# Kernel optimization log

Measured on AMD Instinct MI355X. Metric: run time of the kernel, lower is better.

The kernel has to match this reference:

```python
import jax, jax.numpy as jnp
import numpy as np

B, N, DIM = 2, 2048, 2048
HEADS, DIM_HEAD = 16, 64
INNER = HEADS * DIM_HEAD  # 1024, != DIM -> to_out projection active
SCALE = DIM_HEAD ** -0.5


def setup_inputs() -> dict:
    key = jax.random.key(0)
    ks = jax.random.split(key, 10)
    s_in = 1.0 / np.sqrt(DIM)
    s_out = 1.0 / np.sqrt(INNER)
    return {
        "h_t": jax.random.normal(ks[0], (B, N, DIM), jnp.float32),
        "h_a": jax.random.normal(ks[1], (B, N, DIM), jnp.float32),
        "h_v": jax.random.normal(ks[2], (B, N, DIM), jnp.float32),
        "W_q": jax.random.normal(ks[3], (DIM, INNER), jnp.float32) * s_in,
        "W_k_ta": jax.random.normal(ks[4], (DIM, INNER), jnp.float32) * s_in,
        "W_k_tv": jax.random.normal(ks[5], (DIM, INNER), jnp.float32) * s_in,
        "W_v_ta": jax.random.normal(ks[6], (DIM, INNER), jnp.float32) * s_in,
        "W_v_tv": jax.random.normal(ks[7], (DIM, INNER), jnp.float32) * s_in,
        "W_out": jax.random.normal(ks[8], (INNER, DIM), jnp.float32) * s_out,
        "b_out": jnp.zeros((DIM,), jnp.float32),
    }


def _split_heads(x):
    # [b, n, h*d] -> [b, h, n, d]
    b, n, _ = x.shape
    return x.reshape(b, n, HEADS, DIM_HEAD).transpose(0, 2, 1, 3)


def _cross_attn(q, k, v):
    # q,k,v: [b, h, n, d]
    dots = jnp.einsum('bhid,bhjd->bhij', q, k) * SCALE
    attn = jax.nn.softmax(dots, axis=-1)
    out = jnp.einsum('bhij,bhjd->bhid', attn, v)
    b, h, n, d = out.shape
    return out.transpose(0, 2, 1, 3).reshape(b, n, h * d)  # [b, n, h*d]


def reference(h_t, h_a, h_v, W_q, W_k_ta, W_k_tv, W_v_ta, W_v_tv, W_out, b_out):
    q = _split_heads(h_t @ W_q)
    k_ta = _split_heads(h_a @ W_k_ta)
    v_ta = _split_heads(h_a @ W_v_ta)
    k_tv = _split_heads(h_v @ W_k_tv)
    v_tv = _split_heads(h_v @ W_v_tv)
    out_ta = _cross_attn(q, k_ta, v_ta)
    out_tv = _cross_attn(q, k_tv, v_tv)
    # project_out=True since inner_dim != dim; dropout=0 (eval)
    return h_t + (out_ta + out_tv) @ W_out + b_out
```

## Files before the change

kernel.cpp:

```cpp
#include <hip/hip_runtime.h>
#include <hip/hip_bf16.h>

typedef __attribute__((ext_vector_type(8))) short s16x8;
typedef __attribute__((ext_vector_type(4))) float f32x4;
typedef unsigned short u16;
typedef unsigned int u32;
typedef unsigned long long u64;

__device__ __forceinline__ u16 f2bf(float x) {
  __hip_bfloat16 h = __float2bfloat16(x);
  return *reinterpret_cast<u16*>(&h);
}
__device__ __forceinline__ float bf2f(u16 x) {
  union { u32 u; float f; } c; c.u = ((u32)x) << 16; return c.f;
}
__device__ __forceinline__ u32 pk2(float lo, float hi) {
  return ((u32)f2bf(hi) << 16) | (u32)f2bf(lo);
}

__device__ __forceinline__ void glds16(const void* g, void* lds) {
  __builtin_amdgcn_global_load_lds(
      (const __attribute__((address_space(1))) u32*)(u64)g,
      (__attribute__((address_space(3))) u32*)(u32)(u64)lds, 16, 0, 0);
}

__device__ __forceinline__ void tcast_tile(const float* __restrict__ in,
                                           u16* __restrict__ out,
                                           int R, int C, int ldo,
                                           int bx, int by, int tid,
                                           u16 (*t)[72]) {
  const int c0 = bx * 64, r0 = by * 64;
#pragma unroll
  for (int it = 0; it < 4; ++it) {
    int c = it * 256 + tid;
    int row = c >> 4, sub = c & 15;
    float4 v = *(const float4*)(in + (u64)(r0 + row) * C + c0 + sub * 4);
    t[sub * 4 + 0][row] = f2bf(v.x);
    t[sub * 4 + 1][row] = f2bf(v.y);
    t[sub * 4 + 2][row] = f2bf(v.z);
    t[sub * 4 + 3][row] = f2bf(v.w);
  }
  __syncthreads();
#pragma unroll
  for (int it = 0; it < 2; ++it) {
    int c = it * 256 + tid;
    int orow = c >> 3, osub = c & 7;
    *(s16x8*)(out + (u64)(c0 + orow) * ldo + r0 + osub * 8) =
        *(const s16x8*)&t[orow][osub * 8];
  }
}

__global__ __launch_bounds__(256) void k_prep(
    const float* __restrict__ h_t, const float* __restrict__ h_a,
    const float* __restrict__ h_v, const float* __restrict__ W_q,
    const float* __restrict__ W_k_ta, const float* __restrict__ W_v_ta,
    const float* __restrict__ W_k_tv, const float* __restrict__ W_v_tv,
    const float* __restrict__ W_out, u16* __restrict__ hT,
    u16* __restrict__ hA, u16* __restrict__ hV, u16* __restrict__ WqT,
    u16* __restrict__ WkvTa, u16* __restrict__ WkvTv, u16* __restrict__ WoT) {
  __shared__ u16 t[64][72];
  const int bid = blockIdx.x, tid = threadIdx.x;
  if (bid < 12288) {
    const float* in = bid < 4096 ? h_t : bid < 8192 ? h_a : h_v;
    u16* out = bid < 4096 ? hT : bid < 8192 ? hA : hV;
    const int i = (bid & 4095) * 2048 + tid * 8;
    float4 a = *(const float4*)(in + i);
    float4 b = *(const float4*)(in + i + 4);
    union { s16x8 v; u16 e[8]; } r;
    r.e[0] = f2bf(a.x); r.e[1] = f2bf(a.y); r.e[2] = f2bf(a.z); r.e[3] = f2bf(a.w);
    r.e[4] = f2bf(b.x); r.e[5] = f2bf(b.y); r.e[6] = f2bf(b.z); r.e[7] = f2bf(b.w);
    *(s16x8*)(out + i) = r.v;
  } else if (bid < 14848) {
    const int tt = bid - 12288;
    const int wi = tt / 512, t2 = tt % 512;
    const float* in;
    u16* out;
    switch (wi) {
      case 0: in = W_q;    out = WqT; break;
      case 1: in = W_k_ta; out = WkvTa; break;
      case 2: in = W_v_ta; out = WkvTa + 1024 * 2048; break;
      case 3: in = W_k_tv; out = WkvTv; break;
      default: in = W_v_tv; out = WkvTv + 1024 * 2048; break;
    }
    tcast_tile(in, out, 2048, 1024, 2048, t2 % 16, t2 / 16, tid, t);
  } else {
    const int t2 = bid - 14848;
    tcast_tile(W_out, WoT, 1024, 2048, 1024, t2 % 32, t2 / 32, tid, t);
  }
}

__global__ __launch_bounds__(256) void k_vtrans2(const u16* __restrict__ kva,
                                                 const u16* __restrict__ kvv,
                                                 u16* __restrict__ vta,
                                                 u16* __restrict__ vtv) {
  __shared__ u16 t[64][72];
  const int bx = blockIdx.x, tb = blockIdx.y;
  const int bh = bx & 31;
  const u16* kv = (bx < 32) ? kva : kvv;
  u16* vt = (bx < 32) ? vta : vtv;
  const int b = bh >> 4, h = bh & 15;
  const int tid = threadIdx.x;
  const u16* src = kv + (u64)(b * 2048 + tb * 64) * 2048 + 1024 + h * 64;
#pragma unroll
  for (int it = 0; it < 2; ++it) {
    int c = it * 256 + tid;
    int trow = c >> 3, dsub = c & 7;
    union { s16x8 v; u16 e[8]; } u;
    u.v = *(const s16x8*)(src + (u64)trow * 2048 + dsub * 8);
#pragma unroll
    for (int j = 0; j < 8; ++j) t[dsub * 8 + j][trow] = u.e[j];
  }
  __syncthreads();
  u16* dst = vt + (u64)bh * 64 * 2048 + tb * 64;
#pragma unroll
  for (int it = 0; it < 2; ++it) {
    int c = it * 256 + tid;
    int drow = c >> 3, tsub = c & 7;
    *(s16x8*)(dst + (u64)drow * 2048 + tsub * 8) = *(const s16x8*)&t[drow][tsub * 8];
  }
}

__global__ __launch_bounds__(256) void k_add(const u16* __restrict__ ao,
                                             u16* __restrict__ aoc) {
  const int i = blockIdx.x * 2048 + threadIdx.x * 8;
  const int row = i >> 10, col = i & 1023;
  union { s16x8 v; u16 e[8]; } A, B, O;
  A.v = *(const s16x8*)(ao + (u64)row * 2048 + col);
  B.v = *(const s16x8*)(ao + (u64)row * 2048 + 1024 + col);
#pragma unroll
  for (int j = 0; j < 8; ++j) O.e[j] = f2bf(bf2f(A.e[j]) + bf2f(B.e[j]));
  *(s16x8*)(aoc + (u64)row * 1024 + col) = O.v;
}

template <int TM, int TN, int MODE>
__device__ __forceinline__ void gemm_body(const u16* __restrict__ A,
                                          const u16* __restrict__ Bt,
                                          void* __restrict__ Cout,
                                          const float* __restrict__ resid,
                                          const float* __restrict__ bias,
                                          int M, int N, int K, float scale,
                                          int bxx, int byy) {
  constexpr int MR = TM / 32, NR = TN / 32;
  __shared__ u16 smem[(TM + TN) * 64];
  const int tid = threadIdx.x;
  const int lane = tid & 63, w = tid >> 6;
  const int g = lane >> 4, lr = lane & 15;
  const int wm = (w >> 1) * (TM / 2), wn = (w & 1) * (TN / 2);
  const int m0 = byy * TM, n0 = bxx * TN;

  f32x4 acc[MR][NR] = {};
  int roff[2];
  roff[0] = (g * 16) ^ ((lr & 7) << 4);
  roff[1] = (64 + g * 16) ^ ((lr & 7) << 4);

  const int nkt = K >> 6;
  for (int kt = 0; kt < nkt; ++kt) {
    const int k0 = kt << 6;
#pragma unroll
    for (int it = 0; it < (TM + TN) / 32; ++it) {
      int c = it * 256 + tid;
      int p = c * 16;
      const u16* gsrc;
      if (c < TM * 8) {
        int lby = p ^ (((p >> 7) & 7) << 4);
        gsrc = A + (u64)(m0 + (lby >> 7)) * K + k0 + ((lby >> 4) & 7) * 8;
      } else {
        int pb = p - TM * 128;
        int lby = pb ^ (((pb >> 7) & 7) << 4);
        gsrc = Bt + (u64)(n0 + (lby >> 7)) * K + k0 + ((lby >> 4) & 7) * 8;
      }
      glds16(gsrc, (char*)smem + p);
    }
    __syncthreads();
#pragma unroll
    for (int ks = 0; ks < 2; ++ks) {
      s16x8 a[MR], b[NR];
#pragma unroll
      for (int m = 0; m < MR; ++m)
        a[m] = *(const s16x8*)((const char*)smem + (wm + m * 16 + lr) * 128 + roff[ks]);
#pragma unroll
      for (int n = 0; n < NR; ++n)
        b[n] = *(const s16x8*)((const char*)smem + TM * 128 + (wn + n * 16 + lr) * 128 + roff[ks]);
#pragma unroll
      for (int m = 0; m < MR; ++m)
#pragma unroll
        for (int n = 0; n < NR; ++n)
          acc[m][n] = __builtin_amdgcn_mfma_f32_16x16x32_bf16(a[m], b[n], acc[m][n], 0, 0, 0);
    }
    __syncthreads();
  }

#pragma unroll
  for (int m = 0; m < MR; ++m)
#pragma unroll
    for (int n = 0; n < NR; ++n) {
      const int col = n0 + wn + n * 16 + lr;
#pragma unroll
      for (int r = 0; r < 4; ++r) {
        const int row = m0 + wm + m * 16 + g * 4 + r;
        if constexpr (MODE == 0) {
          ((u16*)Cout)[(u64)row * N + col] = f2bf(acc[m][n][r]);
        } else if constexpr (MODE == 2) {
          ((u16*)Cout)[(u64)row * N + col] = f2bf(acc[m][n][r] * scale);
        } else {
          ((float*)Cout)[(u64)row * N + col] =
              acc[m][n][r] + resid[(u64)row * N + col] + bias[col];
        }
      }
    }
}

template <int TM, int TN, int MODE>
__global__ __launch_bounds__(256) void k_gemm(const u16* __restrict__ A,
                                              const u16* __restrict__ Bt,
                                              void* __restrict__ Cout,
                                              const float* __restrict__ resid,
                                              const float* __restrict__ bias,
                                              int M, int N, int K, float scale) {
  gemm_body<TM, TN, MODE>(A, Bt, Cout, resid, bias, M, N, K, scale,
                          blockIdx.x, blockIdx.y);
}

__global__ __launch_bounds__(256) void k_gemm_kv(const u16* __restrict__ A0,
                                                 const u16* __restrict__ A1,
                                                 const u16* __restrict__ B0,
                                                 const u16* __restrict__ B1,
                                                 u16* __restrict__ C0,
                                                 u16* __restrict__ C1) {
  const int z = blockIdx.z;
  gemm_body<128, 128, 0>(z ? A1 : A0, z ? B1 : B0, z ? C1 : C0,
                         nullptr, nullptr, 4096, 2048, 2048, 1.0f,
                         blockIdx.x, blockIdx.y);
}

__global__ __launch_bounds__(512, 6) void k_attn(const u16* __restrict__ Q,
                                                 const u16* __restrict__ Kta,
                                                 const u16* __restrict__ Ktv,
                                                 const u16* __restrict__ VTta,
                                                 const u16* __restrict__ VTtv,
                                                 u16* __restrict__ AO) {
  const int bx = blockIdx.x;
  const int br = bx & 1, bh = bx >> 1;
  const int b = bh >> 4, h = bh & 15;
  const int qb = blockIdx.y;
  const int tid = threadIdx.x, lane = tid & 63, w = tid >> 6;
  const int g = lane >> 4, q = lane & 15;
  const int qrow = b * 2048 + qb * 128 + w * 16;
  const int bh64 = bh * 64;
  const u16* Kp  = br ? Ktv  : Kta;
  const u16* VTp = br ? VTtv : VTta;

  __shared__ __align__(16) char sbuf[2][16384];
  __shared__ u32 pbuf[8][16][32];

  s16x8 qf[2];
#pragma unroll
  for (int ks = 0; ks < 2; ++ks)
    qf[ks] = *(const s16x8*)(Q + (u64)(qrow + q) * 1024 + h * 64 + ks * 32 + g * 8);

  union { s16x8 v; u16 e[8]; } ones;
#pragma unroll
  for (int j = 0; j < 8; ++j) ones.e[j] = 0x3F80;

  const int sp = tid * 16;
  const int slby = sp ^ (((sp >> 7) & 7) << 4);
  const int srow = slby >> 7, scol = (slby & 127) >> 1;

  {
    glds16(Kp + (u64)(b * 2048 + srow) * 2048 + h * 64 + scol, sbuf[0] + sp);
    glds16(VTp + (u64)(bh64 + srow) * 2048 + scol, sbuf[0] + 8192 + sp);
  }
  __syncthreads();

  f32x4 lacc = {};
  f32x4 acco[4] = {};
  const int xsw = (q & 7) << 4;
  const int psw = (q & 7) << 2;

  for (int t = 0; t < 32; ++t) {
    const int cur = t & 1;
    if (t + 1 < 32) {
      const int kv1 = (t + 1) * 64;
      glds16(Kp + (u64)(b * 2048 + kv1 + srow) * 2048 + h * 64 + scol,
             sbuf[cur ^ 1] + sp);
      glds16(VTp + (u64)(bh64 + srow) * 2048 + kv1 + scol,
             sbuf[cur ^ 1] + 8192 + sp);
    }

    f32x4 s[4];
    __builtin_amdgcn_s_setprio(1);
#pragma unroll
    for (int n = 0; n < 4; ++n) {
      const char* base = sbuf[cur] + (16 * n + q) * 128;
      s16x8 kf0 = *(const s16x8*)(base + ((16 * g) ^ xsw));
      s16x8 kf1 = *(const s16x8*)(base + ((64 + 16 * g) ^ xsw));
      f32x4 z = {};
      z = __builtin_amdgcn_mfma_f32_16x16x32_bf16(kf0, qf[0], z, 0, 0, 0);
      s[n] = __builtin_amdgcn_mfma_f32_16x16x32_bf16(kf1, qf[1], z, 0, 0, 0);
    }
    __builtin_amdgcn_s_setprio(0);

#pragma unroll
    for (int n = 0; n < 4; ++n) {
#pragma unroll
      for (int r = 0; r < 4; ++r) s[n][r] = __builtin_amdgcn_exp2f(s[n][r]);
      pbuf[w][q][(8 * n + 2 * g) ^ psw]     = pk2(s[n][0], s[n][1]);
      pbuf[w][q][(8 * n + 2 * g + 1) ^ psw] = pk2(s[n][2], s[n][3]);
    }
    s16x8 pb[2];
#pragma unroll
    for (int ks = 0; ks < 2; ++ks)
      pb[ks] = *(const s16x8*)&pbuf[w][q][(16 * ks + 4 * g) ^ psw];

    __builtin_amdgcn_s_setprio(1);
    lacc = __builtin_amdgcn_mfma_f32_16x16x32_bf16(ones.v, pb[0], lacc, 0, 0, 0);
    lacc = __builtin_amdgcn_mfma_f32_16x16x32_bf16(ones.v, pb[1], lacc, 0, 0, 0);
#pragma unroll
    for (int n = 0; n < 4; ++n) {
      const char* base = sbuf[cur] + 8192 + (16 * n + q) * 128;
      s16x8 v0 = *(const s16x8*)(base + ((16 * g) ^ xsw));
      s16x8 v1 = *(const s16x8*)(base + ((64 + 16 * g) ^ xsw));
      acco[n] = __builtin_amdgcn_mfma_f32_16x16x32_bf16(v0, pb[0], acco[n], 0, 0, 0);
      acco[n] = __builtin_amdgcn_mfma_f32_16x16x32_bf16(v1, pb[1], acco[n], 0, 0, 0);
    }
    __builtin_amdgcn_s_setprio(0);
    __syncthreads();
  }

  const float inv = 1.0f / lacc[0];

#pragma unroll
  for (int n = 0; n < 4; ++n) {
    pbuf[w][q][(8 * n + 2 * g) ^ psw]     = pk2(acco[n][0] * inv, acco[n][1] * inv);
    pbuf[w][q][(8 * n + 2 * g + 1) ^ psw] = pk2(acco[n][2] * inv, acco[n][3] * inv);
  }
#pragma unroll
  for (int c = 0; c < 2; ++c) {
    const int row = (lane >> 3) + 8 * c;
    const int wc = (lane & 7) * 4;
    s16x8 vv = *(const s16x8*)&pbuf[w][row][wc ^ ((row & 7) << 2)];
    *(s16x8*)(AO + (u64)(b * 2048 + qb * 128 + w * 16 + row) * 2048 +
              br * 1024 + h * 64 + (lane & 7) * 8) = vv;
  }
}

extern "C" void kernel_launch(void* const* d_in, const int* in_sizes, int n_in,
                              void* d_out, int out_size, void* d_ws, size_t ws_size,
                              hipStream_t stream) {
  (void)in_sizes; (void)n_in; (void)out_size; (void)ws_size;
  const float* h_t    = (const float*)d_in[0];
  const float* h_a    = (const float*)d_in[1];
  const float* h_v    = (const float*)d_in[2];
  const float* W_q    = (const float*)d_in[3];
  const float* W_k_ta = (const float*)d_in[4];
  const float* W_k_tv = (const float*)d_in[5];
  const float* W_v_ta = (const float*)d_in[6];
  const float* W_v_tv = (const float*)d_in[7];
  const float* W_out  = (const float*)d_in[8];
  const float* b_out  = (const float*)d_in[9];
  float* out = (float*)d_out;

  const float CEXP = 0.125f * 1.44269504088896f;

  u16* ws    = (u16*)d_ws;
  u16* hT    = ws;
  u16* hA    = hT + 8388608;
  u16* hV    = hA + 8388608;
  u16* WqT   = hV + 8388608;
  u16* WkvTa = WqT + 2097152;
  u16* WkvTv = WkvTa + 4194304;
  u16* WoT   = WkvTv + 4194304;
  u16* Qb    = WoT + 2097152;
  u16* KVta  = Qb + 4194304;
  u16* KVtv  = KVta + 8388608;
  u16* VTta  = KVtv + 8388608;
  u16* VTtv  = VTta + 4194304;
  u16* AO    = hT;
  u16* AOc   = hA;

  k_prep<<<15360, 256, 0, stream>>>(h_t, h_a, h_v, W_q, W_k_ta, W_v_ta,
                                    W_k_tv, W_v_tv, W_out,
                                    hT, hA, hV, WqT, WkvTa, WkvTv, WoT);

  k_gemm<64, 128, 2><<<dim3(8, 64), 256, 0, stream>>>(hT, WqT, Qb, nullptr, nullptr, 4096, 1024, 2048, CEXP);
  k_gemm_kv<<<dim3(16, 32, 2), 256, 0, stream>>>(hA, hV, WkvTa, WkvTv, KVta, KVtv);

  k_vtrans2<<<dim3(64, 32), 256, 0, stream>>>(KVta, KVtv, VTta, VTtv);

  k_attn<<<dim3(64, 16), 512, 0, stream>>>(Qb, KVta, KVtv, VTta, VTtv, AO);

  k_add<<<2048, 256, 0, stream>>>(AO, AOc);

  k_gemm<128, 128, 1><<<dim3(16, 32), 256, 0, stream>>>(AOc, WoT, out, h_t, b_out, 4096, 2048, 1024, 1.0f);
}
```

Before: 294.2 us.

## Fuse head-branch sum into output GEMM and merge Q/KV projection launches

Removes the standalone k_add kernel. The output-projection GEMM (new MODE 3) now loads both branch halves of the attention output, adds them in registers and writes the sum to shared memory, instead of staging a pre-summed buffer through global memory. The Q projection is also folded into the KV projection launch as a third z-slice using 128x128 tiles; the surplus x-blocks of that slice return early. This saves a kernel launch and a global round-trip of the summed buffer. In exchange, the A-operand load in the output GEMM becomes a register load plus add instead of a direct global-to-LDS copy, and the Q GEMM uses larger tiles, which gives fewer blocks.

```diff
diff --git a/kernel.cpp b/kernel.cpp
--- a/kernel.cpp
+++ b/kernel.cpp
@@ -120,18 +120,6 @@
   }
 }
 
-__global__ __launch_bounds__(256) void k_add(const u16* __restrict__ ao,
-                                             u16* __restrict__ aoc) {
-  const int i = blockIdx.x * 2048 + threadIdx.x * 8;
-  const int row = i >> 10, col = i & 1023;
-  union { s16x8 v; u16 e[8]; } A, B, O;
-  A.v = *(const s16x8*)(ao + (u64)row * 2048 + col);
-  B.v = *(const s16x8*)(ao + (u64)row * 2048 + 1024 + col);
-#pragma unroll
-  for (int j = 0; j < 8; ++j) O.e[j] = f2bf(bf2f(A.e[j]) + bf2f(B.e[j]));
-  *(s16x8*)(aoc + (u64)row * 1024 + col) = O.v;
-}
-
 template <int TM, int TN, int MODE>
 __device__ __forceinline__ void gemm_body(const u16* __restrict__ A,
                                           const u16* __restrict__ Bt,
@@ -160,16 +148,26 @@
     for (int it = 0; it < (TM + TN) / 32; ++it) {
       int c = it * 256 + tid;
       int p = c * 16;
-      const u16* gsrc;
       if (c < TM * 8) {
         int lby = p ^ (((p >> 7) & 7) << 4);
-        gsrc = A + (u64)(m0 + (lby >> 7)) * K + k0 + ((lby >> 4) & 7) * 8;
+        if constexpr (MODE == 3) {
+          const u16* g0 = A + (u64)(m0 + (lby >> 7)) * 2048 + k0 + ((lby >> 4) & 7) * 8;
+          union { s16x8 v; u16 e[8]; } a0, a1, r;
+          a0.v = *(const s16x8*)g0;
+          a1.v = *(const s16x8*)(g0 + 1024);
+#pragma unroll
+          for (int j = 0; j < 8; ++j) r.e[j] = f2bf(bf2f(a0.e[j]) + bf2f(a1.e[j]));
+          *(s16x8*)((char*)smem + p) = r.v;
+        } else {
+          glds16(A + (u64)(m0 + (lby >> 7)) * K + k0 + ((lby >> 4) & 7) * 8,
+                 (char*)smem + p);
+        }
       } else {
         int pb = p - TM * 128;
         int lby = pb ^ (((pb >> 7) & 7) << 4);
-        gsrc = Bt + (u64)(n0 + (lby >> 7)) * K + k0 + ((lby >> 4) & 7) * 8;
+        glds16(Bt + (u64)(n0 + (lby >> 7)) * K + k0 + ((lby >> 4) & 7) * 8,
+               (char*)smem + p);
       }
-      glds16(gsrc, (char*)smem + p);
     }
     __syncthreads();
 #pragma unroll
@@ -221,16 +219,24 @@
                           blockIdx.x, blockIdx.y);
 }
 
-__global__ __launch_bounds__(256) void k_gemm_kv(const u16* __restrict__ A0,
-                                                 const u16* __restrict__ A1,
-                                                 const u16* __restrict__ B0,
-                                                 const u16* __restrict__ B1,
-                                                 u16* __restrict__ C0,
-                                                 u16* __restrict__ C1) {
+__global__ __launch_bounds__(256) void k_gemm_qkv(
+    const u16* __restrict__ hT, const u16* __restrict__ hA,
+    const u16* __restrict__ hV, const u16* __restrict__ WqT,
+    const u16* __restrict__ WkvTa, const u16* __restrict__ WkvTv,
+    u16* __restrict__ Qb, u16* __restrict__ KVta, u16* __restrict__ KVtv,
+    float cexp) {
   const int z = blockIdx.z;
-  gemm_body<128, 128, 0>(z ? A1 : A0, z ? B1 : B0, z ? C1 : C0,
-                         nullptr, nullptr, 4096, 2048, 2048, 1.0f,
-                         blockIdx.x, blockIdx.y);
+  if (z == 0) {
+    if (blockIdx.x >= 8) return;
+    gemm_body<128, 128, 2>(hT, WqT, Qb, nullptr, nullptr,
+                           4096, 1024, 2048, cexp, blockIdx.x, blockIdx.y);
+  } else if (z == 1) {
+    gemm_body<128, 128, 0>(hA, WkvTa, KVta, nullptr, nullptr,
+                           4096, 2048, 2048, 1.0f, blockIdx.x, blockIdx.y);
+  } else {
+    gemm_body<128, 128, 0>(hV, WkvTv, KVtv, nullptr, nullptr,
+                           4096, 2048, 2048, 1.0f, blockIdx.x, blockIdx.y);
+  }
 }
 
 __global__ __launch_bounds__(512, 6) void k_attn(const u16* __restrict__ Q,
@@ -376,20 +382,17 @@
   u16* VTta  = KVtv + 8388608;
   u16* VTtv  = VTta + 4194304;
   u16* AO    = hT;
-  u16* AOc   = hA;
 
   k_prep<<<15360, 256, 0, stream>>>(h_t, h_a, h_v, W_q, W_k_ta, W_v_ta,
                                     W_k_tv, W_v_tv, W_out,
                                     hT, hA, hV, WqT, WkvTa, WkvTv, WoT);
 
-  k_gemm<64, 128, 2><<<dim3(8, 64), 256, 0, stream>>>(hT, WqT, Qb, nullptr, nullptr, 4096, 1024, 2048, CEXP);
-  k_gemm_kv<<<dim3(16, 32, 2), 256, 0, stream>>>(hA, hV, WkvTa, WkvTv, KVta, KVtv);
+  k_gemm_qkv<<<dim3(16, 32, 3), 256, 0, stream>>>(hT, hA, hV, WqT, WkvTa,
+                                                  WkvTv, Qb, KVta, KVtv, CEXP);
 
   k_vtrans2<<<dim3(64, 32), 256, 0, stream>>>(KVta, KVtv, VTta, VTtv);
 
   k_attn<<<dim3(64, 16), 512, 0, stream>>>(Qb, KVta, KVtv, VTta, VTtv, AO);
 
-  k_add<<<2048, 256, 0, stream>>>(AO, AOc);
-
-  k_gemm<128, 128, 1><<<dim3(16, 32), 256, 0, stream>>>(AOc, WoT, out, h_t, b_out, 4096, 2048, 1024, 1.0f);
-}
+  k_gemm<128, 128, 3><<<dim3(16, 32), 256, 0, stream>>>(AO, WoT, out, h_t, b_out, 4096, 2048, 1024, 1.0f);
+}
```

Result: slower. 309.3 us (+5.1%).

## Compute transposed V directly via swapped-operand GEMM, dropping the transpose kernel

Applied to the files above, without the earlier changes.

The fused K/V projection GEMM is split in two. K is computed alone into a compact 1024-wide buffer, and V^T is produced directly by a second GEMM that swaps operands (W_v^T times h^T), writing with a new per-batch output layout. This removes the separate V transpose kernel and its extra write and read of the V activations. The attention kernel's K stride is updated to match. The cost is one more GEMM launch, and the V^T GEMM now stores with a different write pattern.

```diff
diff --git a/kernel.cpp b/kernel.cpp
--- a/kernel.cpp
+++ b/kernel.cpp
@@ -89,37 +89,6 @@
   }
 }
 
-__global__ __launch_bounds__(256) void k_vtrans2(const u16* __restrict__ kva,
-                                                 const u16* __restrict__ kvv,
-                                                 u16* __restrict__ vta,
-                                                 u16* __restrict__ vtv) {
-  __shared__ u16 t[64][72];
-  const int bx = blockIdx.x, tb = blockIdx.y;
-  const int bh = bx & 31;
-  const u16* kv = (bx < 32) ? kva : kvv;
-  u16* vt = (bx < 32) ? vta : vtv;
-  const int b = bh >> 4, h = bh & 15;
-  const int tid = threadIdx.x;
-  const u16* src = kv + (u64)(b * 2048 + tb * 64) * 2048 + 1024 + h * 64;
-#pragma unroll
-  for (int it = 0; it < 2; ++it) {
-    int c = it * 256 + tid;
-    int trow = c >> 3, dsub = c & 7;
-    union { s16x8 v; u16 e[8]; } u;
-    u.v = *(const s16x8*)(src + (u64)trow * 2048 + dsub * 8);
-#pragma unroll
-    for (int j = 0; j < 8; ++j) t[dsub * 8 + j][trow] = u.e[j];
-  }
-  __syncthreads();
-  u16* dst = vt + (u64)bh * 64 * 2048 + tb * 64;
-#pragma unroll
-  for (int it = 0; it < 2; ++it) {
-    int c = it * 256 + tid;
-    int drow = c >> 3, tsub = c & 7;
-    *(s16x8*)(dst + (u64)drow * 2048 + tsub * 8) = *(const s16x8*)&t[drow][tsub * 8];
-  }
-}
-
 __global__ __launch_bounds__(256) void k_add(const u16* __restrict__ ao,
                                              u16* __restrict__ aoc) {
   const int i = blockIdx.x * 2048 + threadIdx.x * 8;
@@ -202,6 +171,10 @@
           ((u16*)Cout)[(u64)row * N + col] = f2bf(acc[m][n][r]);
         } else if constexpr (MODE == 2) {
           ((u16*)Cout)[(u64)row * N + col] = f2bf(acc[m][n][r] * scale);
+        } else if constexpr (MODE == 4) {
+          const int bb = col >> 11;
+          ((u16*)Cout)[(u64)bb * 2097152 + (u64)row * 2048 + (col & 2047)] =
+              f2bf(acc[m][n][r]);
         } else {
           ((float*)Cout)[(u64)row * N + col] =
               acc[m][n][r] + resid[(u64)row * N + col] + bias[col];
@@ -221,15 +194,27 @@
                           blockIdx.x, blockIdx.y);
 }
 
-__global__ __launch_bounds__(256) void k_gemm_kv(const u16* __restrict__ A0,
+__global__ __launch_bounds__(256) void k_gemm_k(const u16* __restrict__ A0,
+                                                const u16* __restrict__ A1,
+                                                const u16* __restrict__ B0,
+                                                const u16* __restrict__ B1,
+                                                u16* __restrict__ C0,
+                                                u16* __restrict__ C1) {
+  const int z = blockIdx.z;
+  gemm_body<128, 128, 0>(z ? A1 : A0, z ? B1 : B0, z ? C1 : C0,
+                         nullptr, nullptr, 4096, 1024, 2048, 1.0f,
+                         blockIdx.x, blockIdx.y);
+}
+
+__global__ __launch_bounds__(256) void k_gemm_vt(const u16* __restrict__ A0,
                                                  const u16* __restrict__ A1,
                                                  const u16* __restrict__ B0,
                                                  const u16* __restrict__ B1,
                                                  u16* __restrict__ C0,
                                                  u16* __restrict__ C1) {
   const int z = blockIdx.z;
-  gemm_body<128, 128, 0>(z ? A1 : A0, z ? B1 : B0, z ? C1 : C0,
-                         nullptr, nullptr, 4096, 2048, 2048, 1.0f,
+  gemm_body<128, 128, 4>(z ? A1 : A0, z ? B1 : B0, z ? C1 : C0,
+                         nullptr, nullptr, 1024, 4096, 2048, 1.0f,
                          blockIdx.x, blockIdx.y);
 }
 
@@ -267,7 +252,7 @@
   const int srow = slby >> 7, scol = (slby & 127) >> 1;
 
   {
-    glds16(Kp + (u64)(b * 2048 + srow) * 2048 + h * 64 + scol, sbuf[0] + sp);
+    glds16(Kp + (u64)(b * 2048 + srow) * 1024 + h * 64 + scol, sbuf[0] + sp);
     glds16(VTp + (u64)(bh64 + srow) * 2048 + scol, sbuf[0] + 8192 + sp);
   }
   __syncthreads();
@@ -281,7 +266,7 @@
     const int cur = t & 1;
     if (t + 1 < 32) {
       const int kv1 = (t + 1) * 64;
-      glds16(Kp + (u64)(b * 2048 + kv1 + srow) * 2048 + h * 64 + scol,
+      glds16(Kp + (u64)(b * 2048 + kv1 + srow) * 1024 + h * 64 + scol,
              sbuf[cur ^ 1] + sp);
       glds16(VTp + (u64)(bh64 + srow) * 2048 + kv1 + scol,
              sbuf[cur ^ 1] + 8192 + sp);
@@ -371,9 +356,9 @@
   u16* WkvTv = WkvTa + 4194304;
   u16* WoT   = WkvTv + 4194304;
   u16* Qb    = WoT + 2097152;
-  u16* KVta  = Qb + 4194304;
-  u16* KVtv  = KVta + 8388608;
-  u16* VTta  = KVtv + 8388608;
+  u16* Kta   = Qb + 4194304;
+  u16* Ktv   = Kta + 4194304;
+  u16* VTta  = Ktv + 4194304;
   u16* VTtv  = VTta + 4194304;
   u16* AO    = hT;
   u16* AOc   = hA;
@@ -383,11 +368,13 @@
                                     hT, hA, hV, WqT, WkvTa, WkvTv, WoT);
 
   k_gemm<64, 128, 2><<<dim3(8, 64), 256, 0, stream>>>(hT, WqT, Qb, nullptr, nullptr, 4096, 1024, 2048, CEXP);
-  k_gemm_kv<<<dim3(16, 32, 2), 256, 0, stream>>>(hA, hV, WkvTa, WkvTv, KVta, KVtv);
-
-  k_vtrans2<<<dim3(64, 32), 256, 0, stream>>>(KVta, KVtv, VTta, VTtv);
-
-  k_attn<<<dim3(64, 16), 512, 0, stream>>>(Qb, KVta, KVtv, VTta, VTtv, AO);
+
+  k_gemm_k<<<dim3(8, 32, 2), 256, 0, stream>>>(hA, hV, WkvTa, WkvTv, Kta, Ktv);
+
+  k_gemm_vt<<<dim3(32, 8, 2), 256, 0, stream>>>(WkvTa + 1024 * 2048, WkvTv + 1024 * 2048,
+                                                hA, hV, VTta, VTtv);
+
+  k_attn<<<dim3(64, 16), 512, 0, stream>>>(Qb, Kta, Ktv, VTta, VTtv, AO);
 
   k_add<<<2048, 256, 0, stream>>>(AO, AOc);
 
```

Result: slower. 301.4 us (+2.4%).

## Fuse both cross-attention branches into one attention block and drop add kernel

Applied to the files above, without the earlier changes.

Each attention block now loops over both the text-audio and text-video branches in sequence, sums the normalized outputs in registers, and writes the combined bf16 result directly. This removes the separate elementwise add kernel and the round trip of the doubled-width intermediate buffer. The cost is that the grid is halved (512 blocks instead of 1024), so each block runs twice as long and there is less parallelism across the GPU. The running sum is also held in extra registers, which may affect occupancy.

```diff
diff --git a/kernel.cpp b/kernel.cpp
--- a/kernel.cpp
+++ b/kernel.cpp
@@ -120,18 +120,6 @@
   }
 }
 
-__global__ __launch_bounds__(256) void k_add(const u16* __restrict__ ao,
-                                             u16* __restrict__ aoc) {
-  const int i = blockIdx.x * 2048 + threadIdx.x * 8;
-  const int row = i >> 10, col = i & 1023;
-  union { s16x8 v; u16 e[8]; } A, B, O;
-  A.v = *(const s16x8*)(ao + (u64)row * 2048 + col);
-  B.v = *(const s16x8*)(ao + (u64)row * 2048 + 1024 + col);
-#pragma unroll
-  for (int j = 0; j < 8; ++j) O.e[j] = f2bf(bf2f(A.e[j]) + bf2f(B.e[j]));
-  *(s16x8*)(aoc + (u64)row * 1024 + col) = O.v;
-}
-
 template <int TM, int TN, int MODE>
 __device__ __forceinline__ void gemm_body(const u16* __restrict__ A,
                                           const u16* __restrict__ Bt,
@@ -238,17 +226,14 @@
                                                  const u16* __restrict__ Ktv,
                                                  const u16* __restrict__ VTta,
                                                  const u16* __restrict__ VTtv,
-                                                 u16* __restrict__ AO) {
-  const int bx = blockIdx.x;
-  const int br = bx & 1, bh = bx >> 1;
+                                                 u16* __restrict__ AOc) {
+  const int bh = blockIdx.x;
   const int b = bh >> 4, h = bh & 15;
   const int qb = blockIdx.y;
   const int tid = threadIdx.x, lane = tid & 63, w = tid >> 6;
   const int g = lane >> 4, q = lane & 15;
   const int qrow = b * 2048 + qb * 128 + w * 16;
   const int bh64 = bh * 64;
-  const u16* Kp  = br ? Ktv  : Kta;
-  const u16* VTp = br ? VTtv : VTta;
 
   __shared__ __align__(16) char sbuf[2][16384];
   __shared__ u32 pbuf[8][16][32];
@@ -266,81 +251,92 @@
   const int slby = sp ^ (((sp >> 7) & 7) << 4);
   const int srow = slby >> 7, scol = (slby & 127) >> 1;
 
-  {
+  const int xsw = (q & 7) << 4;
+  const int psw = (q & 7) << 2;
+
+  f32x4 outf[4] = {};
+
+#pragma unroll 1
+  for (int br = 0; br < 2; ++br) {
+    const u16* Kp  = br ? Ktv  : Kta;
+    const u16* VTp = br ? VTtv : VTta;
+
     glds16(Kp + (u64)(b * 2048 + srow) * 2048 + h * 64 + scol, sbuf[0] + sp);
     glds16(VTp + (u64)(bh64 + srow) * 2048 + scol, sbuf[0] + 8192 + sp);
-  }
-  __syncthreads();
-
-  f32x4 lacc = {};
-  f32x4 acco[4] = {};
-  const int xsw = (q & 7) << 4;
-  const int psw = (q & 7) << 2;
-
-  for (int t = 0; t < 32; ++t) {
-    const int cur = t & 1;
-    if (t + 1 < 32) {
-      const int kv1 = (t + 1) * 64;
-      glds16(Kp + (u64)(b * 2048 + kv1 + srow) * 2048 + h * 64 + scol,
-             sbuf[cur ^ 1] + sp);
-      glds16(VTp + (u64)(bh64 + srow) * 2048 + kv1 + scol,
-             sbuf[cur ^ 1] + 8192 + sp);
-    }
-
-    f32x4 s[4];
-    __builtin_amdgcn_s_setprio(1);
-#pragma unroll
-    for (int n = 0; n < 4; ++n) {
-      const char* base = sbuf[cur] + (16 * n + q) * 128;
-      s16x8 kf0 = *(const s16x8*)(base + ((16 * g) ^ xsw));
-      s16x8 kf1 = *(const s16x8*)(base + ((64 + 16 * g) ^ xsw));
-      f32x4 z = {};
-      z = __builtin_amdgcn_mfma_f32_16x16x32_bf16(kf0, qf[0], z, 0, 0, 0);
-      s[n] = __builtin_amdgcn_mfma_f32_16x16x32_bf16(kf1, qf[1], z, 0, 0, 0);
-    }
-    __builtin_amdgcn_s_setprio(0);
-
-#pragma unroll
-    for (int n = 0; n < 4; ++n) {
-#pragma unroll
-      for (int r = 0; r < 4; ++r) s[n][r] = __builtin_amdgcn_exp2f(s[n][r]);
-      pbuf[w][q][(8 * n + 2 * g) ^ psw]     = pk2(s[n][0], s[n][1]);
-      pbuf[w][q][(8 * n + 2 * g + 1) ^ psw] = pk2(s[n][2], s[n][3]);
-    }
-    s16x8 pb[2];
-#pragma unroll
-    for (int ks = 0; ks < 2; ++ks)
-      pb[ks] = *(const s16x8*)&pbuf[w][q][(16 * ks + 4 * g) ^ psw];
-
-    __builtin_amdgcn_s_setprio(1);
-    lacc = __builtin_amdgcn_mfma_f32_16x16x32_bf16(ones.v, pb[0], lacc, 0, 0, 0);
-    lacc = __builtin_amdgcn_mfma_f32_16x16x32_bf16(ones.v, pb[1], lacc, 0, 0, 0);
-#pragma unroll
-    for (int n = 0; n < 4; ++n) {
-      const char* base = sbuf[cur] + 8192 + (16 * n + q) * 128;
-      s16x8 v0 = *(const s16x8*)(base + ((16 * g) ^ xsw));
-      s16x8 v1 = *(const s16x8*)(base + ((64 + 16 * g) ^ xsw));
-      acco[n] = __builtin_amdgcn_mfma_f32_16x16x32_bf16(v0, pb[0], acco[n], 0, 0, 0);
-      acco[n] = __builtin_amdgcn_mfma_f32_16x16x32_bf16(v1, pb[1], acco[n], 0, 0, 0);
-    }
-    __builtin_amdgcn_s_setprio(0);
     __syncthreads();
-  }
-
-  const float inv = 1.0f / lacc[0];
+
+    f32x4 lacc = {};
+    f32x4 acco[4] = {};
+
+    for (int t = 0; t < 32; ++t) {
+      const int cur = t & 1;
+      if (t + 1 < 32) {
+        const int kv1 = (t + 1) * 64;
+        glds16(Kp + (u64)(b * 2048 + kv1 + srow) * 2048 + h * 64 + scol,
+               sbuf[cur ^ 1] + sp);
+        glds16(VTp + (u64)(bh64 + srow) * 2048 + kv1 + scol,
+               sbuf[cur ^ 1] + 8192 + sp);
+      }
+
+      f32x4 s[4];
+      __builtin_amdgcn_s_setprio(1);
+#pragma unroll
+      for (int n = 0; n < 4; ++n) {
+        const char* base = sbuf[cur] + (16 * n + q) * 128;
+        s16x8 kf0 = *(const s16x8*)(base + ((16 * g) ^ xsw));
+        s16x8 kf1 = *(const s16x8*)(base + ((64 + 16 * g) ^ xsw));
+        f32x4 z = {};
+        z = __builtin_amdgcn_mfma_f32_16x16x32_bf16(kf0, qf[0], z, 0, 0, 0);
+        s[n] = __builtin_amdgcn_mfma_f32_16x16x32_bf16(kf1, qf[1], z, 0, 0, 0);
+      }
+      __builtin_amdgcn_s_setprio(0);
+
+#pragma unroll
+      for (int n = 0; n < 4; ++n) {
+#pragma unroll
+        for (int r = 0; r < 4; ++r) s[n][r] = __builtin_amdgcn_exp2f(s[n][r]);
+        pbuf[w][q][(8 * n + 2 * g) ^ psw]     = pk2(s[n][0], s[n][1]);
+        pbuf[w][q][(8 * n + 2 * g + 1) ^ psw] = pk2(s[n][2], s[n][3]);
+      }
+      s16x8 pb[2];
+#pragma unroll
+      for (int ks = 0; ks < 2; ++ks)
+        pb[ks] = *(const s16x8*)&pbuf[w][q][(16 * ks + 4 * g) ^ psw];
+
+      __builtin_amdgcn_s_setprio(1);
+      lacc = __builtin_amdgcn_mfma_f32_16x16x32_bf16(ones.v, pb[0], lacc, 0, 0, 0);
+      lacc = __builtin_amdgcn_mfma_f32_16x16x32_bf16(ones.v, pb[1], lacc, 0, 0, 0);
+#pragma unroll
+      for (int n = 0; n < 4; ++n) {
+        const char* base = sbuf[cur] + 8192 + (16 * n + q) * 128;
+        s16x8 v0 = *(const s16x8*)(base + ((16 * g) ^ xsw));
+        s16x8 v1 = *(const s16x8*)(base + ((64 + 16 * g) ^ xsw));
+        acco[n] = __builtin_amdgcn_mfma_f32_16x16x32_bf16(v0, pb[0], acco[n], 0, 0, 0);
+        acco[n] = __builtin_amdgcn_mfma_f32_16x16x32_bf16(v1, pb[1], acco[n], 0, 0, 0);
+      }
+      __builtin_amdgcn_s_setprio(0);
+      __syncthreads();
+    }
+
+    const float inv = 1.0f / lacc[0];
+#pragma unroll
+    for (int n = 0; n < 4; ++n)
+#pragma unroll
+      for (int r = 0; r < 4; ++r) outf[n][r] += acco[n][r] * inv;
+  }
 
 #pragma unroll
   for (int n = 0; n < 4; ++n) {
-    pbuf[w][q][(8 * n + 2 * g) ^ psw]     = pk2(acco[n][0] * inv, acco[n][1] * inv);
-    pbuf[w][q][(8 * n + 2 * g + 1) ^ psw] = pk2(acco[n][2] * inv, acco[n][3] * inv);
+    pbuf[w][q][(8 * n + 2 * g) ^ psw]     = pk2(outf[n][0], outf[n][1]);
+    pbuf[w][q][(8 * n + 2 * g + 1) ^ psw] = pk2(outf[n][2], outf[n][3]);
   }
 #pragma unroll
   for (int c = 0; c < 2; ++c) {
     const int row = (lane >> 3) + 8 * c;
     const int wc = (lane & 7) * 4;
     s16x8 vv = *(const s16x8*)&pbuf[w][row][wc ^ ((row & 7) << 2)];
-    *(s16x8*)(AO + (u64)(b * 2048 + qb * 128 + w * 16 + row) * 2048 +
-              br * 1024 + h * 64 + (lane & 7) * 8) = vv;
+    *(s16x8*)(AOc + (u64)(b * 2048 + qb * 128 + w * 16 + row) * 1024 +
+              h * 64 + (lane & 7) * 8) = vv;
   }
 }
 
@@ -375,7 +371,6 @@
   u16* KVtv  = KVta + 8388608;
   u16* VTta  = KVtv + 8388608;
   u16* VTtv  = VTta + 4194304;
-  u16* AO    = hT;
   u16* AOc   = hA;
 
   k_prep<<<15360, 256, 0, stream>>>(h_t, h_a, h_v, W_q, W_k_ta, W_v_ta,
@@ -387,9 +382,7 @@
 
   k_vtrans2<<<dim3(64, 32), 256, 0, stream>>>(KVta, KVtv, VTta, VTtv);
 
-  k_attn<<<dim3(64, 16), 512, 0, stream>>>(Qb, KVta, KVtv, VTta, VTtv, AO);
-
-  k_add<<<2048, 256, 0, stream>>>(AO, AOc);
+  k_attn<<<dim3(32, 16), 512, 0, stream>>>(Qb, KVta, KVtv, VTta, VTtv, AOc);
 
   k_gemm<128, 128, 1><<<dim3(16, 32), 256, 0, stream>>>(AOc, WoT, out, h_t, b_out, 4096, 2048, 1024, 1.0f);
 }
```

Measured after the change: 310.3 us. 5.5% more time.
